# Performance work log

Measured on AMD Instinct MI355X. Metric: run time of the kernel, lower is better.

The kernel has to match this reference:

```python
import jax, jax.numpy as jnp
import numpy as np

N = 100000          # num nodes
E = 1600000         # num edges
EMB = 192           # embedding_dimension (divisible by 3)
THIRD = EMB // 3    # 64
NUM_REL = 2
SLOPE = 0.01        # LeakyReLU default negative slope


def leaky_relu(x):
    return jnp.where(x >= 0, x, SLOPE * x)


def setup_inputs() -> dict:
    key = jax.random.key(0)
    ks = jax.random.split(key, 20)
    s = 0.02
    inp = {
        "des": jax.random.normal(ks[0], (N, 768), jnp.float32),
        "tweet": jax.random.normal(ks[1], (N, 768), jnp.float32),
        "num_prop": jax.random.normal(ks[2], (N, 4), jnp.float32),
        "cat_prop": jax.random.normal(ks[3], (N, 3), jnp.float32),
        "edge_index": jax.random.randint(ks[4], (2, E), 0, N, jnp.int64).astype(jnp.int32),
        "edge_type": jax.random.randint(ks[5], (E,), 0, NUM_REL, jnp.int32),
        # params
        "W_des": s * jax.random.normal(ks[6], (768, THIRD), jnp.float32),
        "b_des": jnp.zeros((THIRD,), jnp.float32),
        "W_num": s * jax.random.normal(ks[7], (4, THIRD), jnp.float32),
        "b_num": jnp.zeros((THIRD,), jnp.float32),
        "W_cat": s * jax.random.normal(ks[8], (3, THIRD), jnp.float32),
        "b_cat": jnp.zeros((THIRD,), jnp.float32),
        "W_in": s * jax.random.normal(ks[9], (EMB, EMB), jnp.float32),
        "b_in": jnp.zeros((EMB,), jnp.float32),
        "W_root": s * jax.random.normal(ks[10], (EMB, EMB), jnp.float32),
        "W_rel": s * jax.random.normal(ks[11], (NUM_REL, EMB, EMB), jnp.float32),
        "b_rgcn": jnp.zeros((EMB,), jnp.float32),
        "W_o1": s * jax.random.normal(ks[12], (EMB, EMB), jnp.float32),
        "b_o1": jnp.zeros((EMB,), jnp.float32),
        "W_o2": s * jax.random.normal(ks[13], (EMB, 2), jnp.float32),
        "b_o2": jnp.zeros((2,), jnp.float32),
    }
    return inp


def rgcn_conv(x, edge_index, edge_type, W_root, W_rel, b_rgcn):
    # PyG RGCNConv (default): out = x @ W_root + b + sum_r mean_{edges r -> i}(x[src] @ W_r)
    # mean of (x_j @ W_r) == (mean of x_j) @ W_r, so aggregate first (cheaper).
    src, dst = edge_index[0], edge_index[1]
    h = x[src]  # [E, EMB] gather
    out = x @ W_root + b_rgcn
    for r in range(NUM_REL):
        m = (edge_type == r).astype(x.dtype)  # [E]
        s = jax.ops.segment_sum(h * m[:, None], dst, num_segments=N)  # [N, EMB]
        cnt = jax.ops.segment_sum(m, dst, num_segments=N)             # [N]
        agg = s / jnp.maximum(cnt, 1.0)[:, None]
        out = out + agg @ W_rel[r]
    return out


def reference(des, tweet, num_prop, cat_prop, edge_index, edge_type,
              W_des, b_des, W_num, b_num, W_cat, b_cat, W_in, b_in,
              W_root, W_rel, b_rgcn, W_o1, b_o1, W_o2, b_o2):
    d = leaky_relu(des @ W_des + b_des)
    n = leaky_relu(num_prop @ W_num + b_num)
    c = leaky_relu(cat_prop @ W_cat + b_cat)
    x = jnp.concatenate((d, n, c), axis=1)          # [N, EMB]
    x = leaky_relu(x @ W_in + b_in)
    x = rgcn_conv(x, edge_index, edge_type, W_root, W_rel, b_rgcn)
    # dropout in eval mode = identity
    x = rgcn_conv(x, edge_index, edge_type, W_root, W_rel, b_rgcn)
    x = leaky_relu(x @ W_o1 + b_o1)
    x = x @ W_o2 + b_o2                              # [N, 2]
    return x
```

## Files before the change

### kernel.cpp

```cpp
#include <hip/hip_runtime.h>

typedef _Float16 f16;
typedef _Float16 f16x4 __attribute__((ext_vector_type(4)));
typedef _Float16 f16x8 __attribute__((ext_vector_type(8)));
typedef float f32x4 __attribute__((ext_vector_type(4)));

#define LRELU(v) ((v) >= 0.f ? (v) : 0.01f * (v))

__device__ __forceinline__ int swz(int a) { return a ^ (((a >> 7) & 7) << 4); }

__global__ __launch_bounds__(256) void zero_cursor(int* __restrict__ cursor, int N)
{
  int i = blockIdx.x * 256 + threadIdx.x;
  if (i < N) cursor[i] = 0;
}

__global__ __launch_bounds__(256) void prep_w(
    const float* __restrict__ W_des, const float* __restrict__ W_in,
    const float* __restrict__ W_root, const float* __restrict__ W_rel,
    const float* __restrict__ W_o1,
    f16* __restrict__ WtDes, f16* __restrict__ WtIn, f16* __restrict__ WtR,
    f16* __restrict__ WtO1)
{
  int which = blockIdx.y;
  int idx = blockIdx.x * 256 + threadIdx.x;
  if (which == 0) {
    if (idx < 64 * 768) { int n = idx / 768, k = idx % 768; WtDes[idx] = (f16)W_des[k * 64 + n]; }
  } else if (which == 1) {
    if (idx < 192 * 192) { int n = idx / 192, k = idx % 192; WtIn[idx] = (f16)W_in[k * 192 + n]; }
  } else if (which == 2) {
    if (idx < 192 * 576) {
      int n = idx / 576, k = idx % 576;
      int seg = k / 192, kk = k % 192;
      float v = (seg == 0) ? W_root[kk * 192 + n] : W_rel[(seg - 1) * 192 * 192 + kk * 192 + n];
      WtR[idx] = (f16)v;
    }
  } else {
    if (idx < 192 * 192) { int n = idx / 192, k = idx % 192; WtO1[idx] = (f16)W_o1[k * 192 + n]; }
  }
}

#define BCAP 64
__global__ __launch_bounds__(256) void count_fill(
    const int* __restrict__ ei, const int* __restrict__ et,
    int* __restrict__ cursor, int* __restrict__ bucket, int E)
{
  int e = blockIdx.x * 256 + threadIdx.x;
  if (e >= E) return;
  int src = ei[e];
  int dst = ei[E + e];
  int r = et[e];
  int pos = atomicAdd(&cursor[dst], 1);
  if (pos < BCAP) bucket[(size_t)dst * BCAP + pos] = src | (r << 31);
}

__global__ __launch_bounds__(256) void feat_small(
    const float* __restrict__ num_prop, const float* __restrict__ cat_prop,
    const float* __restrict__ W_num, const float* __restrict__ b_num,
    const float* __restrict__ W_cat, const float* __restrict__ b_cat,
    f16* __restrict__ x0, int N)
{
  int w = (blockIdx.x * 256 + threadIdx.x) >> 6;
  int lane = threadIdx.x & 63;
  if (w >= N) return;
  const float* npr = num_prop + (size_t)w * 4;
  const float* cpr = cat_prop + (size_t)w * 3;
  float vn = b_num[lane];
#pragma unroll
  for (int k = 0; k < 4; k++) vn += npr[k] * W_num[k * 64 + lane];
  float vc = b_cat[lane];
#pragma unroll
  for (int k = 0; k < 3; k++) vc += cpr[k] * W_cat[k * 64 + lane];
  vn = LRELU(vn);
  vc = LRELU(vc);
  x0[(size_t)w * 192 + 64 + lane] = (f16)vn;
  x0[(size_t)w * 192 + 128 + lane] = (f16)vc;
}

__global__ __launch_bounds__(256) void gemm_des_kernel(
    const float* __restrict__ A, const f16* __restrict__ Bt,
    const float* __restrict__ bias, f16* __restrict__ C, int M)
{
  __shared__ f16 lA[128 * 64];
  __shared__ f16 lB[64 * 64];
  const int tid = threadIdx.x, lane = tid & 63, wid = tid >> 6;
  const int wm = wid >> 1, wn = wid & 1;
  const int m0 = blockIdx.x * 128;
  f32x4 acc[4][2] = {};
  const int arow = tid >> 1, ahalf = tid & 1;
  int agr = m0 + arow;
  if (agr >= M) agr = M - 1;
  const float* asrc = A + (size_t)agr * 768 + ahalf * 32;
  for (int k0 = 0; k0 < 768; k0 += 64) {
    {
      const float4* s4 = reinterpret_cast<const float4*>(asrc + k0);
#pragma unroll
      for (int i = 0; i < 4; i++) {
        float4 u = s4[2 * i], w = s4[2 * i + 1];
        f16x8 h;
        h[0] = (f16)u.x; h[1] = (f16)u.y; h[2] = (f16)u.z; h[3] = (f16)u.w;
        h[4] = (f16)w.x; h[5] = (f16)w.y; h[6] = (f16)w.z; h[7] = (f16)w.w;
        int boff = arow * 128 + ahalf * 64 + i * 16;
        *reinterpret_cast<f16x8*>((char*)lA + swz(boff)) = h;
      }
    }
    {
#pragma unroll
      for (int i = 0; i < 2; i++) {
        int c = tid + i * 256;
        int n = c >> 3, k8 = c & 7;
        f16x8 h = *reinterpret_cast<const f16x8*>(Bt + (size_t)n * 768 + k0 + k8 * 8);
        *reinterpret_cast<f16x8*>((char*)lB + swz(n * 128 + k8 * 16)) = h;
      }
    }
    __syncthreads();
#pragma unroll
    for (int ks = 0; ks < 2; ks++) {
      f16x8 af[4], bf[2];
#pragma unroll
      for (int fm = 0; fm < 4; fm++) {
        int row = wm * 64 + fm * 16 + (lane & 15);
        af[fm] = *reinterpret_cast<const f16x8*>((const char*)lA + swz(row * 128 + ks * 64 + (lane >> 4) * 16));
      }
#pragma unroll
      for (int fn = 0; fn < 2; fn++) {
        int nn = wn * 32 + fn * 16 + (lane & 15);
        bf[fn] = *reinterpret_cast<const f16x8*>((const char*)lB + swz(nn * 128 + ks * 64 + (lane >> 4) * 16));
      }
#pragma unroll
      for (int fm = 0; fm < 4; fm++)
#pragma unroll
        for (int fn = 0; fn < 2; fn++)
          acc[fm][fn] = __builtin_amdgcn_mfma_f32_16x16x32_f16(af[fm], bf[fn], acc[fm][fn], 0, 0, 0);
    }
    __syncthreads();
  }
#pragma unroll
  for (int fm = 0; fm < 4; fm++) {
#pragma unroll
    for (int fn = 0; fn < 2; fn++) {
      int gc = wn * 32 + fn * 16 + (lane & 15);
      float b = bias[gc];
#pragma unroll
      for (int r = 0; r < 4; r++) {
        int gr = m0 + wm * 64 + fm * 16 + (lane >> 4) * 4 + r;
        if (gr < M) {
          float v = acc[fm][fn][r] + b;
          C[(size_t)gr * 192 + gc] = (f16)LRELU(v);
        }
      }
    }
  }
}

template <int NSEG, bool RELU>
__global__ __launch_bounds__(512) void gemm_x_kernel(
    const f16* __restrict__ A0, const f16* __restrict__ A1, const f16* __restrict__ A2,
    const f16* __restrict__ Bt, const float* __restrict__ bias,
    f16* __restrict__ C, int M)
{
  __shared__ f16 lA[128 * 64];
  __shared__ f16 lB[192 * 64];
  const int tid = threadIdx.x, lane = tid & 63, wid = tid >> 6;
  const int wm = wid >> 2, wn = wid & 3;
  const int m0 = blockIdx.x * 128;
  const int Ktot = NSEG * 192;
  f32x4 acc[4][3] = {};
  const f16* segs[3] = {A0, A1, A2};
  const int arow = tid >> 2, aq = tid & 3;
  int agr = m0 + arow;
  if (agr >= M) agr = M - 1;
  int seg = 0, kin = 0;
  for (int it = 0; it < NSEG * 3; it++) {
    {
      const f16x8* s8 = reinterpret_cast<const f16x8*>(segs[seg] + (size_t)agr * 192 + kin + aq * 16);
      f16x8 h0 = s8[0], h1 = s8[1];
      int b0 = arow * 128 + aq * 32;
      *reinterpret_cast<f16x8*>((char*)lA + swz(b0)) = h0;
      *reinterpret_cast<f16x8*>((char*)lA + swz(b0 + 16)) = h1;
    }
    {
      int kb = it * 64;
#pragma unroll
      for (int i = 0; i < 3; i++) {
        int c = tid + i * 512;
        int n = c >> 3, k8 = c & 7;
        f16x8 h = *reinterpret_cast<const f16x8*>(Bt + (size_t)n * Ktot + kb + k8 * 8);
        *reinterpret_cast<f16x8*>((char*)lB + swz(n * 128 + k8 * 16)) = h;
      }
    }
    __syncthreads();
#pragma unroll
    for (int ks = 0; ks < 2; ks++) {
      f16x8 af[4], bf[3];
#pragma unroll
      for (int fm = 0; fm < 4; fm++) {
        int row = wm * 64 + fm * 16 + (lane & 15);
        af[fm] = *reinterpret_cast<const f16x8*>((const char*)lA + swz(row * 128 + ks * 64 + (lane >> 4) * 16));
      }
#pragma unroll
      for (int fn = 0; fn < 3; fn++) {
        int nn = wn * 48 + fn * 16 + (lane & 15);
        bf[fn] = *reinterpret_cast<const f16x8*>((const char*)lB + swz(nn * 128 + ks * 64 + (lane >> 4) * 16));
      }
#pragma unroll
      for (int fm = 0; fm < 4; fm++)
#pragma unroll
        for (int fn = 0; fn < 3; fn++)
          acc[fm][fn] = __builtin_amdgcn_mfma_f32_16x16x32_f16(af[fm], bf[fn], acc[fm][fn], 0, 0, 0);
    }
    __syncthreads();
    kin += 64;
    if (kin == 192) { kin = 0; if (seg < NSEG - 1) seg++; }
  }
#pragma unroll
  for (int fm = 0; fm < 4; fm++) {
#pragma unroll
    for (int fn = 0; fn < 3; fn++) {
      int gc = wn * 48 + fn * 16 + (lane & 15);
      float b = bias[gc];
#pragma unroll
      for (int r = 0; r < 4; r++) {
        int gr = m0 + wm * 64 + fm * 16 + (lane >> 4) * 4 + r;
        if (gr < M) {
          float v = acc[fm][fn][r] + b;
          if (RELU) v = LRELU(v);
          C[(size_t)gr * 192 + gc] = (f16)v;
        }
      }
    }
  }
}

__global__ __launch_bounds__(256) void agg_kernel(
    const f16* __restrict__ x, const int* __restrict__ bucket,
    const int* __restrict__ cursor,
    f16* __restrict__ agg0, f16* __restrict__ agg1, int N)
{
  int w = (blockIdx.x << 2) + (threadIdx.x >> 6);
  if (w >= N) return;
  const int lane = threadIdx.x & 63;
  const int g = lane >> 4, sub = lane & 15;
  int deg = cursor[w];
  if (deg > BCAP) deg = BCAP;
  const int4* bk4 = reinterpret_cast<const int4*>(bucket + (size_t)w * BCAP);
  int4 ee[4];
#pragma unroll
  for (int j = 0; j < 4; ++j) ee[j] = bk4[j * 4 + g];
  float a0[12] = {}, a1[12] = {};
  float c1 = 0.f;
#pragma unroll
  for (int j = 0; j < 4; ++j) {
#pragma unroll
    for (int i = 0; i < 4; ++i) {
      int idx = j * 16 + g * 4 + i;
      if (idx < deg) {
        int e = (i == 0) ? ee[j].x : (i == 1) ? ee[j].y : (i == 2) ? ee[j].z : ee[j].w;
        int src = e & 0x7fffffff;
        const f16* rowp = x + (size_t)src * 192 + sub * 4;
        f16x4 v0 = *reinterpret_cast<const f16x4*>(rowp);
        f16x4 v1 = *reinterpret_cast<const f16x4*>(rowp + 64);
        f16x4 v2 = *reinterpret_cast<const f16x4*>(rowp + 128);
        float f[12];
#pragma unroll
        for (int c = 0; c < 4; ++c) {
          f[c] = (float)v0[c]; f[4 + c] = (float)v1[c]; f[8 + c] = (float)v2[c];
        }
        if (e < 0) {
          c1 += 1.f;
#pragma unroll
          for (int c = 0; c < 12; ++c) a1[c] += f[c];
        } else {
#pragma unroll
          for (int c = 0; c < 12; ++c) a0[c] += f[c];
        }
      }
    }
  }
#pragma unroll
  for (int c = 0; c < 12; ++c) {
    a0[c] += __shfl_xor(a0[c], 16); a0[c] += __shfl_xor(a0[c], 32);
    a1[c] += __shfl_xor(a1[c], 16); a1[c] += __shfl_xor(a1[c], 32);
  }
  c1 += __shfl_xor(c1, 16); c1 += __shfl_xor(c1, 32);
  float c0 = (float)deg - c1;
  float i0 = 1.f / fmaxf(c0, 1.f);
  float i1 = 1.f / fmaxf(c1, 1.f);
  if (g == 0) {
    f16x4 o0[3], o1[3];
#pragma unroll
    for (int c = 0; c < 12; ++c) {
      o0[c >> 2][c & 3] = (f16)(a0[c] * i0);
      o1[c >> 2][c & 3] = (f16)(a1[c] * i1);
    }
#pragma unroll
    for (int c = 0; c < 3; ++c) {
      *reinterpret_cast<f16x4*>(agg0 + (size_t)w * 192 + c * 64 + sub * 4) = o0[c];
      *reinterpret_cast<f16x4*>(agg1 + (size_t)w * 192 + c * 64 + sub * 4) = o1[c];
    }
  }
}

__global__ __launch_bounds__(256) void out_kernel(
    const f16* __restrict__ x, const float* __restrict__ W_o2,
    const float* __restrict__ b_o2, float* __restrict__ out, int N)
{
  int w = (blockIdx.x * 256 + threadIdx.x) >> 6;
  int lane = threadIdx.x & 63;
  if (w >= N) return;
  const f16* row = x + (size_t)w * 192;
  float p0 = 0, p1 = 0;
#pragma unroll
  for (int c = 0; c < 3; c++) {
    int j = lane + c * 64;
    float v = (float)row[j];
    p0 += v * W_o2[j * 2 + 0];
    p1 += v * W_o2[j * 2 + 1];
  }
#pragma unroll
  for (int off = 32; off; off >>= 1) {
    p0 += __shfl_xor(p0, off);
    p1 += __shfl_xor(p1, off);
  }
  if (lane == 0) {
    out[(size_t)w * 2 + 0] = p0 + b_o2[0];
    out[(size_t)w * 2 + 1] = p1 + b_o2[1];
  }
}

extern "C" void kernel_launch(void* const* d_in, const int* in_sizes, int n_in,
                              void* d_out, int out_size, void* d_ws, size_t ws_size,
                              hipStream_t stream)
{
  const float* des      = (const float*)d_in[0];
  const float* num_prop = (const float*)d_in[2];
  const float* cat_prop = (const float*)d_in[3];
  const int* edge_index = (const int*)d_in[4];
  const int* edge_type  = (const int*)d_in[5];
  const float* W_des = (const float*)d_in[6];
  const float* b_des = (const float*)d_in[7];
  const float* W_num = (const float*)d_in[8];
  const float* b_num = (const float*)d_in[9];
  const float* W_cat = (const float*)d_in[10];
  const float* b_cat = (const float*)d_in[11];
  const float* W_in  = (const float*)d_in[12];
  const float* b_in  = (const float*)d_in[13];
  const float* W_root= (const float*)d_in[14];
  const float* W_rel = (const float*)d_in[15];
  const float* b_rgcn= (const float*)d_in[16];
  const float* W_o1  = (const float*)d_in[17];
  const float* b_o1  = (const float*)d_in[18];
  const float* W_o2  = (const float*)d_in[19];
  const float* b_o2  = (const float*)d_in[20];
  float* out = (float*)d_out;

  const int N = in_sizes[2] / 4;
  const int E = in_sizes[5];
  (void)n_in; (void)out_size; (void)ws_size;

  char* base = (char*)d_ws;
  size_t off = 0;
  auto take = [&](size_t bytes) -> void* {
    void* p = base + off;
    off += (bytes + 255) & ~(size_t)255;
    return p;
  };
  f16* xA     = (f16*)take((size_t)N * 192 * 2);
  f16* xB     = (f16*)take((size_t)N * 192 * 2);
  f16* agg0   = (f16*)take((size_t)N * 192 * 2);
  f16* agg1   = (f16*)take((size_t)N * 192 * 2);
  int* bucket = (int*)take((size_t)N * BCAP * 4);
  int* cursor = (int*)take((size_t)N * 4);
  f16* WtDes  = (f16*)take(64 * 768 * 2);
  f16* WtIn   = (f16*)take(192 * 192 * 2);
  f16* WtR    = (f16*)take(192 * 576 * 2);
  f16* WtO1   = (f16*)take(192 * 192 * 2);

  zero_cursor<<<(N + 255) / 256, 256, 0, stream>>>(cursor, N);
  prep_w<<<dim3(432, 4), 256, 0, stream>>>(W_des, W_in, W_root, W_rel, W_o1,
                                           WtDes, WtIn, WtR, WtO1);
  count_fill<<<(E + 255) / 256, 256, 0, stream>>>(edge_index, edge_type, cursor, bucket, E);
  feat_small<<<(N + 3) / 4, 256, 0, stream>>>(num_prop, cat_prop, W_num, b_num, W_cat, b_cat, xA, N);
  gemm_des_kernel<<<(N + 127) / 128, 256, 0, stream>>>(des, WtDes, b_des, xA, N);
  gemm_x_kernel<1, true><<<(N + 127) / 128, 512, 0, stream>>>(xA, xA, xA, WtIn, b_in, xB, N);
  agg_kernel<<<(N + 3) / 4, 256, 0, stream>>>(xB, bucket, cursor, agg0, agg1, N);
  gemm_x_kernel<3, false><<<(N + 127) / 128, 512, 0, stream>>>(xB, agg0, agg1, WtR, b_rgcn, xA, N);
  agg_kernel<<<(N + 3) / 4, 256, 0, stream>>>(xA, bucket, cursor, agg0, agg1, N);
  gemm_x_kernel<3, false><<<(N + 127) / 128, 512, 0, stream>>>(xA, agg0, agg1, WtR, b_rgcn, xB, N);
  gemm_x_kernel<1, true><<<(N + 127) / 128, 512, 0, stream>>>(xB, xB, xB, WtO1, b_o1, xA, N);
  out_kernel<<<(N + 3) / 4, 256, 0, stream>>>(xA, W_o2, b_o2, out, N);
}
```

Baseline: 587.1 us.

## Fuse setup kernels, fold final projection into GEMM epilogue, bound agg loop

Merges zero_cursor, prep_w and feat_small into one setup kernel that dispatches on block index. It also fuses the final 192x2 output projection into the epilogue of the last GEMM, using shuffle reductions and shared-memory atomics, so the O1 activation is never written to or reread from global memory. The aggregation kernel now loops only over the 16-edge groups actually present instead of preloading all four bucket vectors. Together these cut launches, an N x 192 f16 round trip, and wasted bucket loads, at the cost of extra LDS atomics and a sync in the GEMM epilogue.

```diff
diff --git a/kernel.cpp b/kernel.cpp
--- a/kernel.cpp
+++ b/kernel.cpp
@@ -9,38 +9,77 @@
 
 __device__ __forceinline__ int swz(int a) { return a ^ (((a >> 7) & 7) << 4); }
 
-__global__ __launch_bounds__(256) void zero_cursor(int* __restrict__ cursor, int N)
-{
-  int i = blockIdx.x * 256 + threadIdx.x;
-  if (i < N) cursor[i] = 0;
-}
-
-__global__ __launch_bounds__(256) void prep_w(
+#define BCAP 64
+
+__global__ __launch_bounds__(256) void setup_kernel(
+    const float* __restrict__ num_prop, const float* __restrict__ cat_prop,
+    const float* __restrict__ W_num, const float* __restrict__ b_num,
+    const float* __restrict__ W_cat, const float* __restrict__ b_cat,
     const float* __restrict__ W_des, const float* __restrict__ W_in,
     const float* __restrict__ W_root, const float* __restrict__ W_rel,
     const float* __restrict__ W_o1,
+    f16* __restrict__ x0, int* __restrict__ cursor,
     f16* __restrict__ WtDes, f16* __restrict__ WtIn, f16* __restrict__ WtR,
-    f16* __restrict__ WtO1)
-{
-  int which = blockIdx.y;
-  int idx = blockIdx.x * 256 + threadIdx.x;
-  if (which == 0) {
+    f16* __restrict__ WtO1,
+    int N, int nbf, int nbz)
+{
+  int b = blockIdx.x;
+  int tid = threadIdx.x;
+  if (b < nbf) {
+    int w = (b * 256 + tid) >> 6;
+    int lane = tid & 63;
+    if (w < N) {
+      const float* npr = num_prop + (size_t)w * 4;
+      const float* cpr = cat_prop + (size_t)w * 3;
+      float vn = b_num[lane];
+#pragma unroll
+      for (int k = 0; k < 4; k++) vn += npr[k] * W_num[k * 64 + lane];
+      float vc = b_cat[lane];
+#pragma unroll
+      for (int k = 0; k < 3; k++) vc += cpr[k] * W_cat[k * 64 + lane];
+      vn = LRELU(vn);
+      vc = LRELU(vc);
+      x0[(size_t)w * 192 + 64 + lane] = (f16)vn;
+      x0[(size_t)w * 192 + 128 + lane] = (f16)vc;
+    }
+    return;
+  }
+  b -= nbf;
+  if (b < nbz) {
+    int i = b * 256 + tid;
+    if (i < N) cursor[i] = 0;
+    return;
+  }
+  b -= nbz;
+  if (b < 192) {
+    int idx = b * 256 + tid;
     if (idx < 64 * 768) { int n = idx / 768, k = idx % 768; WtDes[idx] = (f16)W_des[k * 64 + n]; }
-  } else if (which == 1) {
+    return;
+  }
+  b -= 192;
+  if (b < 144) {
+    int idx = b * 256 + tid;
     if (idx < 192 * 192) { int n = idx / 192, k = idx % 192; WtIn[idx] = (f16)W_in[k * 192 + n]; }
-  } else if (which == 2) {
+    return;
+  }
+  b -= 144;
+  if (b < 432) {
+    int idx = b * 256 + tid;
     if (idx < 192 * 576) {
       int n = idx / 576, k = idx % 576;
       int seg = k / 192, kk = k % 192;
       float v = (seg == 0) ? W_root[kk * 192 + n] : W_rel[(seg - 1) * 192 * 192 + kk * 192 + n];
       WtR[idx] = (f16)v;
     }
-  } else {
+    return;
+  }
+  b -= 432;
+  {
+    int idx = b * 256 + tid;
     if (idx < 192 * 192) { int n = idx / 192, k = idx % 192; WtO1[idx] = (f16)W_o1[k * 192 + n]; }
   }
 }
 
-#define BCAP 64
 __global__ __launch_bounds__(256) void count_fill(
     const int* __restrict__ ei, const int* __restrict__ et,
     int* __restrict__ cursor, int* __restrict__ bucket, int E)
@@ -52,29 +91,6 @@
   int r = et[e];
   int pos = atomicAdd(&cursor[dst], 1);
   if (pos < BCAP) bucket[(size_t)dst * BCAP + pos] = src | (r << 31);
-}
-
-__global__ __launch_bounds__(256) void feat_small(
-    const float* __restrict__ num_prop, const float* __restrict__ cat_prop,
-    const float* __restrict__ W_num, const float* __restrict__ b_num,
-    const float* __restrict__ W_cat, const float* __restrict__ b_cat,
-    f16* __restrict__ x0, int N)
-{
-  int w = (blockIdx.x * 256 + threadIdx.x) >> 6;
-  int lane = threadIdx.x & 63;
-  if (w >= N) return;
-  const float* npr = num_prop + (size_t)w * 4;
-  const float* cpr = cat_prop + (size_t)w * 3;
-  float vn = b_num[lane];
-#pragma unroll
-  for (int k = 0; k < 4; k++) vn += npr[k] * W_num[k * 64 + lane];
-  float vc = b_cat[lane];
-#pragma unroll
-  for (int k = 0; k < 3; k++) vc += cpr[k] * W_cat[k * 64 + lane];
-  vn = LRELU(vn);
-  vc = LRELU(vc);
-  x0[(size_t)w * 192 + 64 + lane] = (f16)vn;
-  x0[(size_t)w * 192 + 128 + lane] = (f16)vc;
 }
 
 __global__ __launch_bounds__(256) void gemm_des_kernel(
@@ -153,11 +169,13 @@
   }
 }
 
-template <int NSEG, bool RELU>
+template <int NSEG, bool RELU, bool OUT2>
 __global__ __launch_bounds__(512) void gemm_x_kernel(
     const f16* __restrict__ A0, const f16* __restrict__ A1, const f16* __restrict__ A2,
     const f16* __restrict__ Bt, const float* __restrict__ bias,
-    f16* __restrict__ C, int M)
+    f16* __restrict__ C, int M,
+    const float* __restrict__ W_o2, const float* __restrict__ b_o2,
+    float* __restrict__ out)
 {
   __shared__ f16 lA[128 * 64];
   __shared__ f16 lB[192 * 64];
@@ -213,19 +231,59 @@
     kin += 64;
     if (kin == 192) { kin = 0; if (seg < NSEG - 1) seg++; }
   }
-#pragma unroll
-  for (int fm = 0; fm < 4; fm++) {
+  if (OUT2) {
+    __shared__ float red[128][2];
+    for (int i = tid; i < 256; i += 512) ((float*)red)[i] = 0.f;
+    __syncthreads();
+    float bb[3], w2v[3][2];
 #pragma unroll
     for (int fn = 0; fn < 3; fn++) {
       int gc = wn * 48 + fn * 16 + (lane & 15);
-      float b = bias[gc];
+      bb[fn] = bias[gc];
+      w2v[fn][0] = W_o2[gc * 2 + 0];
+      w2v[fn][1] = W_o2[gc * 2 + 1];
+    }
+#pragma unroll
+    for (int fm = 0; fm < 4; fm++) {
 #pragma unroll
       for (int r = 0; r < 4; r++) {
-        int gr = m0 + wm * 64 + fm * 16 + (lane >> 4) * 4 + r;
-        if (gr < M) {
-          float v = acc[fm][fn][r] + b;
-          if (RELU) v = LRELU(v);
-          C[(size_t)gr * 192 + gc] = (f16)v;
+        float p0 = 0.f, p1 = 0.f;
+#pragma unroll
+        for (int fn = 0; fn < 3; fn++) {
+          float v = acc[fm][fn][r] + bb[fn];
+          v = LRELU(v);
+          p0 += v * w2v[fn][0];
+          p1 += v * w2v[fn][1];
+        }
+#pragma unroll
+        for (int m = 1; m < 16; m <<= 1) { p0 += __shfl_xor(p0, m); p1 += __shfl_xor(p1, m); }
+        if ((lane & 15) == 0) {
+          int lr = wm * 64 + fm * 16 + (lane >> 4) * 4 + r;
+          atomicAdd(&red[lr][0], p0);
+          atomicAdd(&red[lr][1], p1);
+        }
+      }
+    }
+    __syncthreads();
+    if (tid < 256) {
+      int gr = m0 + (tid >> 1);
+      if (gr < M) out[(size_t)gr * 2 + (tid & 1)] = red[tid >> 1][tid & 1] + b_o2[tid & 1];
+    }
+  } else {
+#pragma unroll
+    for (int fm = 0; fm < 4; fm++) {
+#pragma unroll
+      for (int fn = 0; fn < 3; fn++) {
+        int gc = wn * 48 + fn * 16 + (lane & 15);
+        float b = bias[gc];
+#pragma unroll
+        for (int r = 0; r < 4; r++) {
+          int gr = m0 + wm * 64 + fm * 16 + (lane >> 4) * 4 + r;
+          if (gr < M) {
+            float v = acc[fm][fn][r] + b;
+            if (RELU) v = LRELU(v);
+            C[(size_t)gr * 192 + gc] = (f16)v;
+          }
         }
       }
     }
@@ -244,18 +302,16 @@
   int deg = cursor[w];
   if (deg > BCAP) deg = BCAP;
   const int4* bk4 = reinterpret_cast<const int4*>(bucket + (size_t)w * BCAP);
-  int4 ee[4];
-#pragma unroll
-  for (int j = 0; j < 4; ++j) ee[j] = bk4[j * 4 + g];
   float a0[12] = {}, a1[12] = {};
   float c1 = 0.f;
-#pragma unroll
-  for (int j = 0; j < 4; ++j) {
+  int nj = (deg + 15) >> 4;
+  for (int j = 0; j < nj; ++j) {
+    int4 ee = bk4[j * 4 + g];
 #pragma unroll
     for (int i = 0; i < 4; ++i) {
       int idx = j * 16 + g * 4 + i;
       if (idx < deg) {
-        int e = (i == 0) ? ee[j].x : (i == 1) ? ee[j].y : (i == 2) ? ee[j].z : ee[j].w;
+        int e = (i == 0) ? ee.x : (i == 1) ? ee.y : (i == 2) ? ee.z : ee.w;
         int src = e & 0x7fffffff;
         const f16* rowp = x + (size_t)src * 192 + sub * 4;
         f16x4 v0 = *reinterpret_cast<const f16x4*>(rowp);
@@ -298,33 +354,6 @@
       *reinterpret_cast<f16x4*>(agg0 + (size_t)w * 192 + c * 64 + sub * 4) = o0[c];
       *reinterpret_cast<f16x4*>(agg1 + (size_t)w * 192 + c * 64 + sub * 4) = o1[c];
     }
-  }
-}
-
-__global__ __launch_bounds__(256) void out_kernel(
-    const f16* __restrict__ x, const float* __restrict__ W_o2,
-    const float* __restrict__ b_o2, float* __restrict__ out, int N)
-{
-  int w = (blockIdx.x * 256 + threadIdx.x) >> 6;
-  int lane = threadIdx.x & 63;
-  if (w >= N) return;
-  const f16* row = x + (size_t)w * 192;
-  float p0 = 0, p1 = 0;
-#pragma unroll
-  for (int c = 0; c < 3; c++) {
-    int j = lane + c * 64;
-    float v = (float)row[j];
-    p0 += v * W_o2[j * 2 + 0];
-    p1 += v * W_o2[j * 2 + 1];
-  }
-#pragma unroll
-  for (int off = 32; off; off >>= 1) {
-    p0 += __shfl_xor(p0, off);
-    p1 += __shfl_xor(p1, off);
-  }
-  if (lane == 0) {
-    out[(size_t)w * 2 + 0] = p0 + b_o2[0];
-    out[(size_t)w * 2 + 1] = p1 + b_o2[1];
   }
 }
 
@@ -376,17 +405,23 @@
   f16* WtR    = (f16*)take(192 * 576 * 2);
   f16* WtO1   = (f16*)take(192 * 192 * 2);
 
-  zero_cursor<<<(N + 255) / 256, 256, 0, stream>>>(cursor, N);
-  prep_w<<<dim3(432, 4), 256, 0, stream>>>(W_des, W_in, W_root, W_rel, W_o1,
-                                           WtDes, WtIn, WtR, WtO1);
+  const int nbf = (N + 3) / 4;
+  const int nbz = (N + 255) / 256;
+  const int nsetup = nbf + nbz + 192 + 144 + 432 + 144;
+  setup_kernel<<<nsetup, 256, 0, stream>>>(
+      num_prop, cat_prop, W_num, b_num, W_cat, b_cat,
+      W_des, W_in, W_root, W_rel, W_o1,
+      xA, cursor, WtDes, WtIn, WtR, WtO1, N, nbf, nbz);
   count_fill<<<(E + 255) / 256, 256, 0, stream>>>(edge_index, edge_type, cursor, bucket, E);
-  feat_small<<<(N + 3) / 4, 256, 0, stream>>>(num_prop, cat_prop, W_num, b_num, W_cat, b_cat, xA, N);
   gemm_des_kernel<<<(N + 127) / 128, 256, 0, stream>>>(des, WtDes, b_des, xA, N);
-  gemm_x_kernel<1, true><<<(N + 127) / 128, 512, 0, stream>>>(xA, xA, xA, WtIn, b_in, xB, N);
+  gemm_x_kernel<1, true, false><<<(N + 127) / 128, 512, 0, stream>>>(
+      xA, xA, xA, WtIn, b_in, xB, N, nullptr, nullptr, nullptr);
   agg_kernel<<<(N + 3) / 4, 256, 0, stream>>>(xB, bucket, cursor, agg0, agg1, N);
-  gemm_x_kernel<3, false><<<(N + 127) / 128, 512, 0, stream>>>(xB, agg0, agg1, WtR, b_rgcn, xA, N);
+  gemm_x_kernel<3, false, false><<<(N + 127) / 128, 512, 0, stream>>>(
+      xB, agg0, agg1, WtR, b_rgcn, xA, N, nullptr, nullptr, nullptr);
   agg_kernel<<<(N + 3) / 4, 256, 0, stream>>>(xA, bucket, cursor, agg0, agg1, N);
-  gemm_x_kernel<3, false><<<(N + 127) / 128, 512, 0, stream>>>(xA, agg0, agg1, WtR, b_rgcn, xB, N);
-  gemm_x_kernel<1, true><<<(N + 127) / 128, 512, 0, stream>>>(xB, xB, xB, WtO1, b_o1, xA, N);
-  out_kernel<<<(N + 3) / 4, 256, 0, stream>>>(xA, W_o2, b_o2, out, N);
-}
+  gemm_x_kernel<3, false, false><<<(N + 127) / 128, 512, 0, stream>>>(
+      xA, agg0, agg1, WtR, b_rgcn, xB, N, nullptr, nullptr, nullptr);
+  gemm_x_kernel<1, false, true><<<(N + 127) / 128, 512, 0, stream>>>(
+      xB, xB, xB, WtO1, b_o1, nullptr, N, W_o2, b_o2, out);
+}
```

After: 557.9 us. -5.0%, faster.
